# Kernel tuning notes

Measured on AMD Instinct MI355X. Metric: run time of the kernel, lower is better.

Reference implementation:

```python
import jax, jax.numpy as jnp
import numpy as np
import math

B, T = 8, 16
CODE_NUM = 1024
CODE_SIZE = 48
GRAPH_SIZE = 32
HIDDEN = 150      # hidden_size == t_output_size
T_ATTN = 32       # t_attention_size
DP_ATTN = 32      # DotProductAttention size
OUT = 1024


def _lin(k, fan_in, fan_out):
    s = 1.0 / math.sqrt(fan_in)
    kw, kb = jax.random.split(k)
    W = jax.random.uniform(kw, (fan_in, fan_out), minval=-s, maxval=s, dtype=jnp.float32)
    b = jax.random.uniform(kb, (fan_out,), minval=-s, maxval=s, dtype=jnp.float32)
    return W, b


def setup_inputs():
    key = jax.random.key(0)
    ks = jax.random.split(key, 16)
    u = jax.random.uniform(ks[0], (B, T, CODE_NUM))
    m1 = (u < 0.03).astype(jnp.float32)                   # persistent codes
    m2 = ((u >= 0.03) & (u < 0.05)).astype(jnp.float32)   # emerging neighbor codes
    m3 = ((u >= 0.05) & (u < 0.06)).astype(jnp.float32)   # emerging unrelated codes
    divided = jnp.stack([m1, m2, m3], axis=-1)            # [B,T,N,3], disjoint
    code_x = jnp.clip(m1 + m2 + m3, 0.0, 1.0)             # current-visit codes
    neighbors = ((u >= 0.06) & (u < 0.12)).astype(jnp.float32)
    lens = jax.random.randint(ks[1], (B,), T // 2, T + 1)
    a = (jax.random.uniform(ks[2], (CODE_NUM, CODE_NUM)) < 0.01).astype(jnp.float32)
    adj = a / (a.sum(axis=1, keepdims=True) + 1e-6)
    c_emb = jax.random.normal(ks[3], (CODE_NUM, CODE_SIZE)) * 0.05
    n_emb = jax.random.normal(ks[4], (CODE_NUM, CODE_SIZE)) * 0.05
    u_emb = jax.random.normal(ks[5], (CODE_NUM, GRAPH_SIZE)) * 0.05
    Wg, bg = _lin(ks[6], CODE_SIZE, GRAPH_SIZE)           # GraphLayer dense
    Wi, bi = _lin(ks[7], GRAPH_SIZE, 3 * HIDDEN)          # GRUCell input (r|z|n)
    Wh, bh = _lin(ks[8], HIDDEN, 3 * HIDDEN)              # GRUCell hidden (r|z|n)
    Wq, bq = _lin(ks[9], GRAPH_SIZE, T_ATTN)
    Wk, bk = _lin(ks[10], GRAPH_SIZE, T_ATTN)
    Wv, bv = _lin(ks[11], GRAPH_SIZE, HIDDEN)
    Wd, bd = _lin(ks[12], HIDDEN, DP_ATTN)                # DotProductAttention dense
    context = jax.random.normal(ks[13], (DP_ATTN,)) * 0.1
    Wc, bc = _lin(ks[14], HIDDEN, OUT)                    # Classifier
    return dict(code_x=code_x, divided=divided, neighbors=neighbors, lens=lens,
                adj=adj, c_emb=c_emb, n_emb=n_emb, u_emb=u_emb, Wg=Wg, bg=bg,
                Wi=Wi, bi=bi, Wh=Wh, bh=bh, Wq=Wq, bq=bq, Wk=Wk, bk=bk,
                Wv=Wv, bv=bv, Wd=Wd, bd=bd, context=context, Wc=Wc, bc=bc)


def _forward(code_x, divided, neighbors, lens, adj, c_emb, n_emb, u_emb,
             Wg, bg, Wi, bi, Wh, bh, Wq, bq, Wk, bk, Wv, bv, Wd, bd, context, Wc, bc):
    Bb, Tt, N = code_x.shape
    H = Wh.shape[0]
    NEG = -1e30
    scale = 1.0 / math.sqrt(Wq.shape[1])

    def step(carry, xs):
        h_prev, no_prev = carry                 # [B,N,H], [B,N,G]
        c_t, d_t, n_t, t_idx = xs               # [B,N], [B,N,3], [B,N], scalar
        c = c_t[..., None]
        nb = n_t[..., None]
        # GraphLayer: masked embeddings + one-hop adjacency aggregation
        ce = c * c_emb                           # [B,N,C]
        ne = nb * n_emb
        adj_ce = jnp.einsum('mn,bnc->bmc', adj, ce)
        adj_ne = jnp.einsum('mn,bnc->bmc', adj, ne)
        co = jax.nn.leaky_relu((ce + c * adj_ce + c * adj_ne) @ Wg + bg)      # [B,N,G]
        no = jax.nn.leaky_relu((ne + nb * adj_ne + nb * adj_ce) @ Wg + bg)

        m1 = d_t[..., 0]; m2 = d_t[..., 1]; m3 = d_t[..., 2]
        # TransitionLayer part 1: GRUCell on persistent (m1) codes; h_new starts at 0
        gi = co @ Wi + bi
        gh = h_prev @ Wh + bh
        i_r, i_z, i_n = jnp.split(gi, 3, axis=-1)
        h_r, h_z, h_n = jnp.split(gh, 3, axis=-1)
        r = jax.nn.sigmoid(i_r + h_r)
        z = jax.nn.sigmoid(i_z + h_z)
        n_g = jnp.tanh(i_n + r * h_n)
        h_m1 = (1.0 - z) * n_g + z * h_prev
        h_new = jnp.where(m1[..., None] > 0, h_m1, 0.0)

        # TransitionLayer part 2: single-head attention over emerging (m2|m3) codes, t>0
        m23 = (m2 + m3) > 0
        qrows = jnp.where(m2[..., None] > 0, no_prev,
                          jnp.where(m3[..., None] > 0, u_emb, 0.0))           # [B,N,G]
        q = qrows @ Wq + bq
        k = co @ Wk + bk
        v = qrows @ Wv + bv
        s = jnp.einsum('bia,bja->bij', q, k) * scale
        s = jnp.where(m23[:, None, :], s, NEG)   # keys restricted to m2|m3 set
        h_m23 = jnp.tanh(jnp.einsum('bij,bjh->bih', jax.nn.softmax(s, axis=-1), v))
        use23 = t_idx > 0
        h_new = jnp.where(jnp.logical_and(use23, m23)[..., None], h_m23, h_new)

        # per-step output: max-pool over each active subset (0 if subset empty)
        om1 = jnp.max(jnp.where(m1[..., None] > 0, h_m1, NEG), axis=1)
        om1 = jnp.where(jnp.any(m1 > 0, axis=1)[:, None], om1, 0.0)
        om23 = jnp.max(jnp.where(m23[..., None], h_m23, NEG), axis=1)
        om23 = jnp.where(jnp.logical_and(use23, jnp.any(m23, axis=1))[:, None], om23, 0.0)
        return (h_new, no), om1 + om23

    h0 = jnp.zeros((Bb, N, H), code_x.dtype)
    no0 = jnp.zeros((Bb, N, Wg.shape[1]), code_x.dtype)
    xs = (jnp.moveaxis(code_x, 1, 0), jnp.moveaxis(divided, 1, 0),
          jnp.moveaxis(neighbors, 1, 0), jnp.arange(Tt))
    _, outs = jax.lax.scan(step, (h0, no0), xs)
    outs = jnp.moveaxis(outs, 0, 1)              # [B,T,H]

    # DotProductAttention over (ragged) visit axis
    vu = (outs @ Wd + bd) @ context              # [B,T]
    tmask = jnp.arange(Tt)[None, :] < lens[:, None]
    score = jax.nn.softmax(jnp.where(tmask, vu, NEG), axis=-1)
    pooled = jnp.einsum('bth,bt->bh', outs, score)
    # Classifier (dropout_rate=0 -> identity) with sigmoid activation
    return jax.nn.sigmoid(pooled @ Wc + bc)


def reference(code_x, divided, neighbors, lens, adj, c_emb, n_emb, u_emb,
              Wg, bg, Wi, bi, Wh, bh, Wq, bq, Wk, bk, Wv, bv, Wd, bd, context, Wc, bc):
    return _forward(code_x, divided, neighbors, lens, adj, c_emb, n_emb, u_emb,
                    Wg, bg, Wi, bi, Wh, bh, Wq, bq, Wk, bk, Wv, bv, Wd, bd,
                    context, Wc, bc)
```

## Files before the change

### kernel.cpp

```cpp
#include <hip/hip_runtime.h>

#define Bq   8
#define Tq   16
#define Nq   1024
#define Cq   48
#define Gq   32
#define Hq   150
#define H3q  450
#define TAq  32
#define OUTq 1024
#define BTq  128
#define NBLK (2 * BTq)
#define THREADS 512

#define NC_CAP 128
#define NM_CAP 64
#define NACT   (2 * NC_CAP)
#define MTILE  16
#define NMH    (NM_CAP / 2)
#define CHUNK  16

__device__ __forceinline__ float lrelu(float x){ return x > 0.f ? x : 0.01f * x; }
__device__ __forceinline__ float sigm(float x){ return 1.f / (1.f + expf(-x)); }

__device__ __align__(16) int   g_n1[BTq], g_n23[BTq], g_nchain[BTq], g_nchain2[BTq];
__device__ __align__(16) int   g_list1[BTq][NM_CAP];
__device__ __align__(16) int   g_list23[BTq][NM_CAP];
__device__ __align__(16) int   g_mapc[BTq][Nq];
__device__ __align__(16) int   g_mapn[BTq][Nq];
__device__ __align__(16) int   g_chain[BTq][NM_CAP];
__device__ __align__(16) int   g_chain2[BTq][NM_CAP];
__device__ __align__(16) int   g_cls[BTq][NM_CAP];
__device__ __align__(16) float g_co[BTq][NC_CAP][Gq];
__device__ __align__(16) float g_no[BTq][NC_CAP][Gq];
__device__ __align__(16) float g_hm23[BTq][NM_CAP][Hq];
__device__ __align__(16) float g_om23p2[2][BTq][Hq];
__device__ __align__(16) float g_hm1[BTq][NM_CAP][Hq];
__device__ __align__(16) float g_om1p2[2][BTq][Hq];
__device__ __align__(16) float g_om1c[BTq][Hq];

template<typename T>
__device__ __forceinline__ T gld(const T* p){
    return __hip_atomic_load(p, __ATOMIC_RELAXED, __HIP_MEMORY_SCOPE_AGENT);
}
template<typename T>
__device__ __forceinline__ void gst(T* p, T v){
    __hip_atomic_store(p, v, __ATOMIC_RELAXED, __HIP_MEMORY_SCOPE_AGENT);
}

__device__ unsigned int g_done[NBLK][16];

__device__ __forceinline__ void publish(unsigned int val){
    asm volatile("s_waitcnt vmcnt(0)" ::: "memory");
    __syncthreads();
    if (threadIdx.x == 0)
        __hip_atomic_store(&g_done[blockIdx.x][0], val,
                           __ATOMIC_RELAXED, __HIP_MEMORY_SCOPE_AGENT);
}

__device__ __forceinline__ void spin_ge(int b2, unsigned int tgt){
    while ((int)(__hip_atomic_load(&g_done[b2][0],
                                   __ATOMIC_RELAXED, __HIP_MEMORY_SCOPE_AGENT) - tgt) < 0)
        __builtin_amdgcn_s_sleep(4);
}

__device__ __forceinline__ void gi3(const float* co_row, const float* Wi, const float* bi, int h,
                                    float& gr, float& gz, float& gn){
    gr = bi[h]; gz = bi[Hq + h]; gn = bi[2 * Hq + h];
    #pragma unroll
    for (int g = 0; g < Gq; ++g){
        float c = co_row[g];
        const float* w = Wi + g * H3q + h;
        gr += c * w[0];
        gz += c * w[Hq];
        gn += c * w[2 * Hq];
    }
}

#define WARM(ptr, nfloats) { int nv_ = (nfloats) >> 2; \
    for (int i4_ = blk * THREADS + tid; i4_ < nv_; i4_ += NBLK * THREADS){ \
        float4 v_ = ((const float4*)(ptr))[i4_]; \
        wacc += v_.x + v_.y + v_.z + v_.w; } }

union SharedU {
    struct {
        unsigned char cf[Nq], nf[Nq];
        short lc[NC_CAP], ln[NC_CAP];
        short act[NACT];
        float Wg[Cq][Gq];
        float Pact[NACT][Gq];
        float A[MTILE][NACT];
    } co;
    struct {
        unsigned char f1[Nq], f2[Nq], f3[Nq];
        short l1[NM_CAP], l23[NM_CAP];
        unsigned char wm[NMH];
        float co23[NM_CAP][Gq];
        float qr[NM_CAP][Gq];
        float q[NMH][TAq + 1];
        float k[NM_CAP][TAq + 1];
        float s[NMH][NM_CAP + 1];
        float vv[NM_CAP][Hq];
        float hm[NMH][Hq];
    } mid;
    struct {
        short map1p[Nq], map23p[Nq];
        short l1[NM_CAP];
        unsigned char cls[NM_CAP];
        int   m23l[NM_CAP];
        float co1[NMH][Gq];
        float hb[Hq];
        float ghf[H3q];
        float gi[NMH][H3q];
    } g1;
    struct {
        int   proc[NM_CAP];
        float hb[CHUNK][Hq];
        float co[CHUNK][Gq];
        float ghf[CHUNK][H3q];
        float hm[CHUNK][Hq];
        float cmax[Hq];
    } g1b;
    struct {
        int   nch2[Tq];
        float co[Gq];
        float hb[Hq];
        float ghf[H3q];
        float outs[Tq][Hq];
        float wdc[Hq];
        float score[Tq];
        float pooled[Hq];
    } fin;
};

#define CO_PREFETCH(P, kk) { int rbase_ = half + (kk) * 2 * MTILE; \
    int ntile_ = min(MTILE, (total - rbase_ + 1) / 2); int lim_ = ntile_ * total; \
    _Pragma("unroll") for (int u = 0; u < 8; ++u){ int idx_ = tid + u * THREADS; \
        if (idx_ < lim_){ int ti_ = idx_ / total, j_ = idx_ - ti_ * total; \
            P[u] = adj[(size_t)sh.co.act[rbase_ + 2 * ti_] * Nq + sh.co.act[j_]]; } } }

#define CO_STORE(P, kk) { int rbase_ = half + (kk) * 2 * MTILE; \
    int ntile_ = min(MTILE, (total - rbase_ + 1) / 2); int lim_ = ntile_ * total; \
    _Pragma("unroll") for (int u = 0; u < 8; ++u){ int idx_ = tid + u * THREADS; \
        if (idx_ < lim_){ int ti_ = idx_ / total, j_ = idx_ - ti_ * total; \
            sh.co.A[ti_][j_] = P[u]; } } }

#define CO_COMPUTE(kk) { int rbase_ = half + (kk) * 2 * MTILE; \
    int ntile_ = min(MTILE, (total - rbase_ + 1) / 2); \
    if (grp < ntile_){ int r_ = rbase_ + 2 * grp; float agg_ = 0.f; \
        _Pragma("unroll 4") for (int j_ = 0; j_ < total; ++j_) \
            agg_ += sh.co.A[grp][j_] * sh.co.Pact[j_][g]; \
        float v_ = lrelu(sh.co.Pact[r_][g] + agg_ + bgv); \
        if (r_ < nc) gst(&g_co[bt][r_][g], v_); else gst(&g_no[bt][r_ - nc][g], v_); } }

__global__ __launch_bounds__(THREADS, 1) void k_fused(
    const float* code_x, const float* divided, const float* neighbors,
    const int* lens, const float* adj, const float* c_emb, const float* n_emb,
    const float* u_emb, const float* Wg, const float* bg,
    const float* Wi, const float* bi, const float* Wh, const float* bh,
    const float* Wq_, const float* bq_, const float* Wk_, const float* bk_,
    const float* Wv_, const float* bv_, const float* Wd, const float* bd,
    const float* ctx, const float* Wc, const float* bc, float* out)
{
    __shared__ SharedU sh;
    __shared__ int s_n0, s_n1v, s_i2;
    const int tid = threadIdx.x;
    const int blk = blockIdx.x;
    const int bt   = blk >> 1;
    const int half = blk & 1;
    const int t    = bt % Tq;
    const int btp  = bt - 1;
    const unsigned int bar0 = __hip_atomic_load(&g_done[blk][0],
                                                __ATOMIC_RELAXED, __HIP_MEMORY_SCOPE_AGENT);

    float wacc = 0.f;
    WARM(code_x,    BTq * Nq);
    WARM(neighbors, BTq * Nq);
    WARM(adj,       Nq * Nq);
    WARM(divided,   BTq * Nq * 3);
    WARM(c_emb,     Nq * Cq);
    WARM(n_emb,     Nq * Cq);
    WARM(u_emb,     Nq * Gq);
    WARM(Wi,        Gq * H3q);
    WARM(Wh,        Hq * H3q);
    WARM(Wc,        Hq * OUTq);
    WARM(Wv_,       Gq * Hq);
    WARM(Wd,        Hq * TAq);
    WARM((const float*)g_co,     BTq * NC_CAP * Gq);
    WARM((const float*)g_no,     BTq * NC_CAP * Gq);
    WARM((const float*)g_hm23,   BTq * NM_CAP * Hq);
    WARM((const float*)g_hm1,    BTq * NM_CAP * Hq);
    WARM((const float*)g_mapc,   BTq * Nq);
    WARM((const float*)g_mapn,   BTq * Nq);
    WARM((const float*)g_om23p2, 2 * BTq * Hq);
    WARM((const float*)g_om1p2,  2 * BTq * Hq);
    WARM((const float*)g_om1c,   BTq * Hq);

    {
        int wave = tid >> 6, lane = tid & 63;
        for (int n = tid; n < Nq; n += THREADS){
            sh.co.cf[n] = (code_x[bt * Nq + n]    > 0.f) ? 1 : 0;
            sh.co.nf[n] = (neighbors[bt * Nq + n] > 0.f) ? 1 : 0;
        }
        for (int i = tid; i < Cq * Gq; i += THREADS) (&sh.co.Wg[0][0])[i] = Wg[i];
        __syncthreads();
        if (wave == 0){
            int base = 0;
            for (int start = 0; start < Nq; start += 64){
                int n = start + lane;
                int pred = sh.co.cf[n];
                unsigned long long mm = __ballot(pred != 0);
                int pos = base + (int)__popcll(mm & ((1ull << lane) - 1ull));
                if (pred && pos < NC_CAP) sh.co.lc[pos] = (short)n;
                base += (int)__popcll(mm);
            }
            if (lane == 0) s_n0 = min(base, NC_CAP);
        } else if (wave == 1){
            int base = 0;
            for (int start = 0; start < Nq; start += 64){
                int n = start + lane;
                int pred = sh.co.nf[n];
                unsigned long long mm = __ballot(pred != 0);
                int pos = base + (int)__popcll(mm & ((1ull << lane) - 1ull));
                if (pred && pos < NC_CAP) sh.co.ln[pos] = (short)n;
                base += (int)__popcll(mm);
            }
            if (lane == 0) s_n1v = min(base, NC_CAP);
        } else {
            if (half == 0) for (int n = tid - 128; n < Nq; n += 384) gst(&g_mapc[bt][n], -1);
            else           for (int n = tid - 128; n < Nq; n += 384) gst(&g_mapn[bt][n], -1);
        }
        __syncthreads();
        int nc = s_n0, nn = s_n1v, total = nc + nn;

        for (int i = tid; i < total; i += THREADS) sh.co.act[i] = (i < nc) ? sh.co.lc[i] : sh.co.ln[i - nc];
        if (half == 0) for (int i = tid; i < nc; i += THREADS) gst(&g_mapc[bt][sh.co.lc[i]], i);
        else           for (int i = tid; i < nn; i += THREADS) gst(&g_mapn[bt][sh.co.ln[i]], i);
        __syncthreads();

        for (int idx = tid; idx < total * Gq; idx += THREADS){
            int i = idx >> 5, g = idx & 31;
            int row = sh.co.act[i];
            const float* e = (i < nc) ? (c_emb + row * Cq) : (n_emb + row * Cq);
            float acc = 0.f;
            #pragma unroll
            for (int c = 0; c < Cq; ++c) acc += e[c] * sh.co.Wg[c][g];
            sh.co.Pact[i][g] = acc;
        }
        __syncthreads();

        int g = tid & 31, grp = tid >> 5;
        float bgv = bg[g];
        int ntiles = (total > half) ? (total - half + 2 * MTILE - 1) / (2 * MTILE) : 0;
        float pA[8], pB[8];
        if (ntiles > 0) CO_PREFETCH(pA, 0);
        for (int k = 0; k < ntiles; ){
            CO_STORE(pA, k);
            __syncthreads();
            if (k + 1 < ntiles) CO_PREFETCH(pB, k + 1);
            CO_COMPUTE(k);
            __syncthreads();
            ++k; if (k >= ntiles) break;
            CO_STORE(pB, k);
            __syncthreads();
            if (k + 1 < ntiles) CO_PREFETCH(pA, k + 1);
            CO_COMPUTE(k);
            __syncthreads();
            ++k;
        }
    }
    asm volatile("" :: "v"(wacc));
    publish(bar0 + 1);
    float dv[6];
    #pragma unroll
    for (int u = 0; u < 6; ++u) dv[u] = divided[(size_t)bt * (Nq * 3) + tid + u * THREADS];
    if (tid == 0) spin_ge(blk ^ 1, bar0 + 1);
    else if (t > 0 && tid == 1) spin_ge(2 * btp,     bar0 + 1);
    else if (t > 0 && tid == 2) spin_ge(2 * btp + 1, bar0 + 1);
    __syncthreads();

    {
        int wave = tid >> 6, lane = tid & 63;
        #pragma unroll
        for (int u = 0; u < 6; ++u){
            int idx = tid + u * THREADS;
            int n = idx / 3, c = idx - n * 3;
            unsigned char f = (dv[u] > 0.f) ? 1 : 0;
            if (c == 0) sh.mid.f1[n] = f;
            else if (c == 1) sh.mid.f2[n] = f;
            else sh.mid.f3[n] = f;
        }
        __syncthreads();
        if (wave == 0){
            int base = 0;
            for (int start = 0; start < Nq; start += 64){
                int n = start + lane;
                int pred = sh.mid.f1[n];
                unsigned long long mm = __ballot(pred != 0);
                int pos = base + (int)__popcll(mm & ((1ull << lane) - 1ull));
                if (pred && pos < NM_CAP) sh.mid.l1[pos] = (short)n;
                base += (int)__popcll(mm);
            }
            if (lane == 0) s_n0 = min(base, NM_CAP);
        } else if (wave == 1){
            int base = 0;
            for (int start = 0; start < Nq; start += 64){
                int n = start + lane;
                int m2 = sh.mid.f2[n], m3 = sh.mid.f3[n];
                int pred = m2 | m3;
                unsigned long long mm = __ballot(pred != 0);
                int pos = base + (int)__popcll(mm & ((1ull << lane) - 1ull));
                if (pred && pos < NM_CAP) sh.mid.l23[pos] = (short)(n | (m2 ? 0x400 : 0));
                base += (int)__popcll(mm);
            }
            if (lane == 0) s_n1v = min(base, NM_CAP);
        }
        __syncthreads();
        int n1 = s_n0, n23 = s_n1v;
        if (half == 0){
            for (int i = tid; i < n1;  i += THREADS) gst(&g_list1[bt][i],  (int)sh.mid.l1[i]);
            for (int i = tid; i < n23; i += THREADS) gst(&g_list23[bt][i], (int)sh.mid.l23[i]);
            if (tid == 0){ gst(&g_n1[bt], n1); gst(&g_n23[bt], n23); }
        }
        if (t != 0 && n23 != 0){
            int nMy = (n23 > half) ? ((n23 - half + 1) >> 1) : 0;

            for (int il = tid; il < nMy; il += THREADS){
                int row = sh.mid.l23[2 * il + half] & 1023;
                unsigned char wmv = 0;
                if (t < Tq - 1) wmv = (divided[((size_t)(bt + 1) * Nq + row) * 3] > 0.f) ? 1 : 0;
                sh.mid.wm[il] = wmv;
            }
            for (int idx = tid; idx < n23 * Gq; idx += THREADS){
                int i = idx >> 5, g = idx & 31;
                sh.mid.co23[i][g] = gld(&g_co[bt][gld(&g_mapc[bt][sh.mid.l23[i] & 1023])][g]);
            }
            for (int idx = tid; idx < n23 * Gq; idx += THREADS){
                int i = idx >> 5, g = idx & 31;
                int e = sh.mid.l23[i], row = e & 1023;
                float qv;
                if (e & 0x400){
                    int slot = gld(&g_mapn[btp][row]);
                    qv = (slot >= 0) ? gld(&g_no[btp][slot][g]) : lrelu(bg[g]);
                } else {
                    qv = u_emb[row * Gq + g];
                }
                sh.mid.qr[i][g] = qv;
            }
            __syncthreads();
            for (int idx = tid; idx < n23 * TAq; idx += THREADS){
                int i = idx >> 5, a = idx & 31;
                float acck = bk_[a];
                #pragma unroll
                for (int g = 0; g < Gq; ++g) acck += sh.mid.co23[i][g] * Wk_[g * TAq + a];
                sh.mid.k[i][a] = acck;
            }
            for (int idx = tid; idx < nMy * TAq; idx += THREADS){
                int il = idx >> 5, a = idx & 31;
                int i = 2 * il + half;
                float accq = bq_[a];
                #pragma unroll
                for (int g = 0; g < Gq; ++g) accq += sh.mid.qr[i][g] * Wq_[g * TAq + a];
                sh.mid.q[il][a] = accq;
            }
            for (int idx = tid; idx < n23 * Hq; idx += THREADS){
                int i = idx / Hq, h = idx % Hq;
                float acc = bv_[h];
                #pragma unroll
                for (int g = 0; g < Gq; ++g) acc += sh.mid.qr[i][g] * Wv_[g * Hq + h];
                sh.mid.vv[i][h] = acc;
            }
            __syncthreads();

            const float scale = 0.17677669529663687f;
            for (int idx = tid; idx < nMy * n23; idx += THREADS){
                int il = idx / n23, j = idx % n23;
                float acc = 0.f;
                #pragma unroll
                for (int a = 0; a < TAq; ++a) acc += sh.mid.q[il][a] * sh.mid.k[j][a];
                sh.mid.s[il][j] = acc * scale;
            }
            __syncthreads();
            for (int il = tid; il < nMy; il += THREADS){
                float mx = -1e30f;
                for (int j = 0; j < n23; ++j) mx = fmaxf(mx, sh.mid.s[il][j]);
                float sum = 0.f;
                for (int j = 0; j < n23; ++j){ float e = expf(sh.mid.s[il][j] - mx); sh.mid.s[il][j] = e; sum += e; }
                float inv = 1.f / sum;
                for (int j = 0; j < n23; ++j) sh.mid.s[il][j] *= inv;
            }
            __syncthreads();
            for (int idx = tid; idx < nMy * Hq; idx += THREADS){
                int il = idx / Hq, h = idx % Hq;
                float acc = 0.f;
                for (int j = 0; j < n23; ++j) acc += sh.mid.s[il][j] * sh.mid.vv[j][h];
                sh.mid.hm[il][h] = tanhf(acc);
            }
            __syncthreads();
            for (int idx = tid; idx < nMy * Hq; idx += THREADS){
                int il = idx / Hq, h = idx % Hq;
                if (sh.mid.wm[il]) gst(&g_hm23[bt][2 * il + half][h], sh.mid.hm[il][h]);
            }
            for (int h = tid; h < Hq; h += THREADS){
                float mx = -1e30f;
                for (int il = 0; il < nMy; ++il) mx = fmaxf(mx, sh.mid.hm[il][h]);
                gst(&g_om23p2[half][bt][h], mx);
            }
        }
    }
    publish(bar0 + 2);
    if (tid == 0) spin_ge(blk ^ 1, bar0 + 2);
    else if (t > 0 && tid == 1) spin_ge(2 * btp,     bar0 + 2);
    else if (t > 0 && tid == 2) spin_ge(2 * btp + 1, bar0 + 2);
    __syncthreads();

    {
        int n1 = gld(&g_n1[bt]);
        int nMy = (n1 > half) ? ((n1 - half + 1) >> 1) : 0;
        for (int n = tid; n < Nq; n += THREADS){
            if (t >= 1) sh.g1.map1p[n] = -1;
            if (t >= 2) sh.g1.map23p[n] = -1;
        }
        for (int i = tid; i < n1; i += THREADS) sh.g1.l1[i] = (short)gld(&g_list1[bt][i]);
        __syncthreads();
        if (t >= 1){
            int n1p = gld(&g_n1[btp]);
            for (int i = tid; i < n1p; i += THREADS) sh.g1.map1p[gld(&g_list1[btp][i])] = (short)i;
            if (t >= 2){
                int n23p = gld(&g_n23[btp]);
                for (int i = tid; i < n23p; i += THREADS) sh.g1.map23p[gld(&g_list23[btp][i]) & 1023] = (short)i;
            }
        }
        __syncthreads();
        if (tid < 64){
            int i = tid;
            int cls = 0, sp = -1;
            if (i < n1 && t >= 1){
                int row = sh.g1.l1[i];
                if (sh.g1.map1p[row] >= 0){ cls = 1; sp = sh.g1.map1p[row]; }
                else if (t >= 2 && sh.g1.map23p[row] >= 0){ cls = 2; sp = sh.g1.map23p[row]; }
            }
            if (i < n1) sh.g1.cls[i] = (unsigned char)cls;
            if (half == 0 && i < n1) gst(&g_cls[bt][i], cls);
            unsigned long long mch = __ballot(cls == 1);
            unsigned long long m23 = __ballot(cls == 2 && (i & 1) == half);
            int pch = (int)__popcll(mch & ((1ull << i) - 1ull));
            int p23 = (int)__popcll(m23 & ((1ull << i) - 1ull));
            if (half == 0 && cls == 1) gst(&g_chain[bt][pch], (i << 16) | sp);
            if (cls == 2 && (i & 1) == half) sh.g1.m23l[p23] = (i << 16) | sp;
            if (i == 0){
                s_i2 = (int)__popcll(m23);
                if (half == 0) gst(&g_nchain[bt], (int)__popcll(mch));
            }
        }
        for (int idx = tid; idx < nMy * Gq; idx += THREADS){
            int il = idx >> 5, g = idx & 31;
            sh.g1.co1[il][g] = gld(&g_co[bt][gld(&g_mapc[bt][sh.g1.l1[2 * il + half]])][g]);
        }
        __syncthreads();

        if (tid < H3q){
            float wcol[Gq];
            #pragma unroll
            for (int g = 0; g < Gq; ++g) wcol[g] = Wi[g * H3q + tid];
            float bij = bi[tid];
            for (int il = 0; il < nMy; ++il){
                float acc = bij;
                #pragma unroll
                for (int g = 0; g < Gq; ++g) acc += sh.g1.co1[il][g] * wcol[g];
                sh.g1.gi[il][tid] = acc;
            }
        }
        __syncthreads();

        for (int idx = tid; idx < nMy * Hq; idx += THREADS){
            int il = idx / Hq, h = idx % Hq;
            int i = 2 * il + half;
            if (sh.g1.cls[i] != 0) continue;
            float gr = sh.g1.gi[il][h], gz = sh.g1.gi[il][Hq + h], gn = sh.g1.gi[il][2 * Hq + h];
            float r  = sigm(gr + bh[h]);
            float z  = sigm(gz + bh[Hq + h]);
            float ng = tanhf(gn + r * bh[2 * Hq + h]);
            sh.g1.gi[il][h] = (1.f - z) * ng;
        }
        __syncthreads();

        int nf23 = s_i2;
        for (int f = 0; f < nf23; ++f){
            int pk = sh.g1.m23l[f]; int i = pk >> 16, sp = pk & 0xffff;
            int il = i >> 1;
            for (int h = tid; h < Hq; h += THREADS) sh.g1.hb[h] = gld(&g_hm23[btp][sp][h]);
            __syncthreads();
            for (int j = tid; j < H3q; j += THREADS){
                float acc = bh[j];
                for (int k2 = 0; k2 < Hq; ++k2) acc += sh.g1.hb[k2] * Wh[k2 * H3q + j];
                sh.g1.ghf[j] = acc;
            }
            __syncthreads();
            for (int h = tid; h < Hq; h += THREADS){
                float gr = sh.g1.gi[il][h], gz = sh.g1.gi[il][Hq + h], gn = sh.g1.gi[il][2 * Hq + h];
                float r  = sigm(gr + sh.g1.ghf[h]);
                float z  = sigm(gz + sh.g1.ghf[Hq + h]);
                float ng = tanhf(gn + r * sh.g1.ghf[2 * Hq + h]);
                sh.g1.gi[il][h] = (1.f - z) * ng + z * sh.g1.hb[h];
            }
            __syncthreads();
        }

        for (int idx = tid; idx < nMy * Hq; idx += THREADS){
            int il = idx / Hq, h = idx % Hq;
            int i = 2 * il + half;
            if (sh.g1.cls[i] != 1) gst(&g_hm1[bt][i][h], sh.g1.gi[il][h]);
        }
        for (int h = tid; h < Hq; h += THREADS){
            float mx = -1e30f;
            for (int il = 0; il < nMy; ++il)
                if (sh.g1.cls[2 * il + half] != 1) mx = fmaxf(mx, sh.g1.gi[il][h]);
            gst(&g_om1p2[half][bt][h], mx);
        }
    }

    if (half == 1){
        publish(bar0 + 5);
        return;
    }
    publish(bar0 + 3);
    if (t > 0){
        if (tid == 0) spin_ge(2 * btp,     bar0 + 3);
        else if (tid == 1) spin_ge(2 * btp + 1, bar0 + 3);
    }
    __syncthreads();

    {
        int nch = (t > 0) ? gld(&g_nchain[bt]) : 0;
        for (int h = tid; h < Hq; h += THREADS) sh.g1b.cmax[h] = -1e30f;
        if (tid < 64){
            int c = tid;
            int pk = 0, defer = 0;
            if (c < nch){
                pk = gld(&g_chain[bt][c]);
                int sp = pk & 0xffff;
                defer = (gld(&g_cls[btp][sp]) == 1) ? 1 : 0;
            }
            unsigned long long md = __ballot((c < nch) && defer);
            unsigned long long mp = __ballot((c < nch) && !defer);
            int pos  = (int)__popcll(md & ((1ull << c) - 1ull));
            int ppos = (int)__popcll(mp & ((1ull << c) - 1ull));
            if ((c < nch) && defer)  gst(&g_chain2[bt][pos], pk);
            if ((c < nch) && !defer) sh.g1b.proc[ppos] = pk;
            if (c == 0){
                gst(&g_nchain2[bt], (int)__popcll(md));
                s_i2 = (int)__popcll(mp);
            }
        }
        __syncthreads();
        int nproc = s_i2;
        for (int cb = 0; cb < nproc; cb += CHUNK){
            int nc2 = min(CHUNK, nproc - cb);
            for (int idx = tid; idx < nc2 * Hq; idx += THREADS){
                int c = idx / Hq, h = idx % Hq;
                int sp = sh.g1b.proc[cb + c] & 0xffff;
                sh.g1b.hb[c][h] = gld(&g_hm1[btp][sp][h]);
            }
            for (int idx = tid; idx < nc2 * Gq; idx += THREADS){
                int c = idx >> 5, g = idx & 31;
                int i = sh.g1b.proc[cb + c] >> 16;
                sh.g1b.co[c][g] = gld(&g_co[bt][gld(&g_mapc[bt][gld(&g_list1[bt][i])])][g]);
            }
            __syncthreads();
            for (int idx = tid; idx < nc2 * H3q; idx += THREADS){
                int c = idx / H3q, j = idx - c * H3q;
                float acc = bh[j];
                for (int k2 = 0; k2 < Hq; ++k2) acc += sh.g1b.hb[c][k2] * Wh[k2 * H3q + j];
                sh.g1b.ghf[c][j] = acc;
            }
            __syncthreads();
            for (int idx = tid; idx < nc2 * Hq; idx += THREADS){
                int c = idx / Hq, h = idx % Hq;
                int i = sh.g1b.proc[cb + c] >> 16;
                float gr, gz, gn;
                gi3(sh.g1b.co[c], Wi, bi, h, gr, gz, gn);
                float r  = sigm(gr + sh.g1b.ghf[c][h]);
                float z  = sigm(gz + sh.g1b.ghf[c][Hq + h]);
                float ng = tanhf(gn + r * sh.g1b.ghf[c][2 * Hq + h]);
                float v  = (1.f - z) * ng + z * sh.g1b.hb[c][h];
                gst(&g_hm1[bt][i][h], v);
                sh.g1b.hm[c][h] = v;
            }
            __syncthreads();
            for (int h = tid; h < Hq; h += THREADS){
                float mx = sh.g1b.cmax[h];
                for (int c = 0; c < nc2; ++c) mx = fmaxf(mx, sh.g1b.hm[c][h]);
                sh.g1b.cmax[h] = mx;
            }
            __syncthreads();
        }
        for (int h = tid; h < Hq; h += THREADS) gst(&g_om1c[bt][h], sh.g1b.cmax[h]);
    }

    if ((blk & 31) != 0){
        publish(bar0 + 5);
        return;
    }
    publish(bar0 + 4);
    {
        int b = blk >> 5;
        if (tid < 32){
            int tt = tid >> 1, par = tid & 1;
            spin_ge(32 * b + 2 * tt + par, par ? (bar0 + 3) : (bar0 + 4));
        }
    }
    __syncthreads();

    {
        int b = blk >> 5;
        if (tid < Tq) sh.fin.nch2[tid] = (tid > 0) ? gld(&g_nchain2[b * Tq + tid]) : 0;
        __syncthreads();
        for (int tt = 1; tt < Tq; ++tt){
            int bt2 = b * Tq + tt, btp2 = bt2 - 1;
            int nch2 = sh.fin.nch2[tt];
            for (int c = 0; c < nch2; ++c){
                int pk = gld(&g_chain2[bt2][c]); int i = pk >> 16, sp = pk & 0xffff;
                if (tid < Gq) sh.fin.co[tid] = gld(&g_co[bt2][gld(&g_mapc[bt2][gld(&g_list1[bt2][i])])][tid]);
                for (int h = tid; h < Hq; h += THREADS) sh.fin.hb[h] = gld(&g_hm1[btp2][sp][h]);
                __syncthreads();
                for (int j = tid; j < H3q; j += THREADS){
                    float acc = bh[j];
                    for (int k2 = 0; k2 < Hq; ++k2) acc += sh.fin.hb[k2] * Wh[k2 * H3q + j];
                    sh.fin.ghf[j] = acc;
                }
                __syncthreads();
                for (int h = tid; h < Hq; h += THREADS){
                    float gr, gz, gn;
                    gi3(sh.fin.co, Wi, bi, h, gr, gz, gn);
                    float r  = sigm(gr + sh.fin.ghf[h]);
                    float z  = sigm(gz + sh.fin.ghf[Hq + h]);
                    float ng = tanhf(gn + r * sh.fin.ghf[2 * Hq + h]);
                    gst(&g_hm1[bt2][i][h], (1.f - z) * ng + z * sh.fin.hb[h]);
                }
                __syncthreads();
            }
        }
        for (int idx = tid; idx < Tq * Hq; idx += THREADS){
            int tt = idx / Hq, h = idx % Hq;
            int bt2 = b * Tq + tt;
            int n1 = gld(&g_n1[bt2]), n23 = (tt > 0) ? gld(&g_n23[bt2]) : 0;
            float o = 0.f;
            if (n1 > 0){
                float mx = fmaxf(fmaxf(gld(&g_om1p2[0][bt2][h]), gld(&g_om1p2[1][bt2][h])),
                                 gld(&g_om1c[bt2][h]));
                int nd = sh.fin.nch2[tt];
                for (int c = 0; c < nd; ++c){
                    int i = gld(&g_chain2[bt2][c]) >> 16;
                    mx = fmaxf(mx, gld(&g_hm1[bt2][i][h]));
                }
                o = mx;
            }
            if (n23 > 0) o += fmaxf(gld(&g_om23p2[0][bt2][h]), gld(&g_om23p2[1][bt2][h]));
            sh.fin.outs[tt][h] = o;
        }
        for (int h = tid; h < Hq; h += THREADS){
            float acc = 0.f;
            for (int d = 0; d < 32; ++d) acc += Wd[h * 32 + d] * ctx[d];
            sh.fin.wdc[h] = acc;
        }
        __syncthreads();
        int len = lens[b];
        if (tid < Tq){
            int tt = tid;
            float acc = 0.f;
            for (int d = 0; d < 32; ++d) acc += bd[d] * ctx[d];
            for (int h = 0; h < Hq; ++h) acc += sh.fin.outs[tt][h] * sh.fin.wdc[h];
            sh.fin.score[tt] = (tt < len) ? acc : -1e30f;
        }
        __syncthreads();
        if (tid == 0){
            float mx = -1e30f;
            for (int tt = 0; tt < Tq; ++tt) mx = fmaxf(mx, sh.fin.score[tt]);
            float sum = 0.f;
            for (int tt = 0; tt < Tq; ++tt){ float e = expf(sh.fin.score[tt] - mx); sh.fin.score[tt] = e; sum += e; }
            float inv = 1.f / sum;
            for (int tt = 0; tt < Tq; ++tt) sh.fin.score[tt] *= inv;
        }
        __syncthreads();
        for (int h = tid; h < Hq; h += THREADS){
            float acc = 0.f;
            for (int tt = 0; tt < Tq; ++tt) acc += sh.fin.score[tt] * sh.fin.outs[tt][h];
            sh.fin.pooled[h] = acc;
        }
        __syncthreads();
        for (int o = tid; o < OUTq; o += THREADS){
            float acc = bc[o];
            for (int h = 0; h < Hq; ++h) acc += sh.fin.pooled[h] * Wc[h * OUTq + o];
            out[b * OUTq + o] = sigm(acc);
        }
    }
    publish(bar0 + 5);
}

extern "C" void kernel_launch(void* const* d_in, const int* in_sizes, int n_in,
                              void* d_out, int out_size, void* d_ws, size_t ws_size,
                              hipStream_t stream){
    const float* code_x    = (const float*)d_in[0];
    const float* divided   = (const float*)d_in[1];
    const float* neighbors = (const float*)d_in[2];
    const int*   lens      = (const int*)  d_in[3];
    const float* adj       = (const float*)d_in[4];
    const float* c_emb     = (const float*)d_in[5];
    const float* n_emb     = (const float*)d_in[6];
    const float* u_emb     = (const float*)d_in[7];
    const float* Wg        = (const float*)d_in[8];
    const float* bg        = (const float*)d_in[9];
    const float* Wi        = (const float*)d_in[10];
    const float* bi        = (const float*)d_in[11];
    const float* Wh        = (const float*)d_in[12];
    const float* bh        = (const float*)d_in[13];
    const float* Wq_       = (const float*)d_in[14];
    const float* bq_       = (const float*)d_in[15];
    const float* Wk_       = (const float*)d_in[16];
    const float* bk_       = (const float*)d_in[17];
    const float* Wv_       = (const float*)d_in[18];
    const float* bv_       = (const float*)d_in[19];
    const float* Wd_       = (const float*)d_in[20];
    const float* bd_       = (const float*)d_in[21];
    const float* ctx       = (const float*)d_in[22];
    const float* Wc_       = (const float*)d_in[23];
    const float* bc_       = (const float*)d_in[24];
    float* out = (float*)d_out;

    hipLaunchKernelGGL(k_fused, dim3(NBLK), dim3(THREADS), 0, stream,
                       code_x, divided, neighbors, lens, adj, c_emb, n_emb, u_emb,
                       Wg, bg, Wi, bi, Wh, bh, Wq_, bq_, Wk_, bk_, Wv_, bv_,
                       Wd_, bd_, ctx, Wc_, bc_, out);
}
```

Before: 237.1 us.

## Distribute final attention and classifier across all blocks per batch

Previously a single block per batch element ran the pooling and the full 1024-wide classifier while the other blocks exited. Now every block of a batch recomputes the attention pooling and produces its own 32-output slice of the classifier, with a split-K reduction through shared memory. The deferred-chain GRU pass stays on the leader block, which publishes a new barrier that the others wait on. Warm-up prefetches of the workspace buffers are also removed. The cost is redundant pooling work in every block and an extra cross-block wait stage.

```diff
diff --git a/kernel.cpp b/kernel.cpp
--- a/kernel.cpp
+++ b/kernel.cpp
@@ -130,6 +130,7 @@
         float wdc[Hq];
         float score[Tq];
         float pooled[Hq];
+        float cpart[32][17];
     } fin;
 };
 
@@ -186,15 +187,6 @@
     WARM(Wc,        Hq * OUTq);
     WARM(Wv_,       Gq * Hq);
     WARM(Wd,        Hq * TAq);
-    WARM((const float*)g_co,     BTq * NC_CAP * Gq);
-    WARM((const float*)g_no,     BTq * NC_CAP * Gq);
-    WARM((const float*)g_hm23,   BTq * NM_CAP * Hq);
-    WARM((const float*)g_hm1,    BTq * NM_CAP * Hq);
-    WARM((const float*)g_mapc,   BTq * Nq);
-    WARM((const float*)g_mapn,   BTq * Nq);
-    WARM((const float*)g_om23p2, 2 * BTq * Hq);
-    WARM((const float*)g_om1p2,  2 * BTq * Hq);
-    WARM((const float*)g_om1c,   BTq * Hq);
 
     {
         int wave = tid >> 6, lane = tid & 63;
@@ -519,128 +511,125 @@
             gst(&g_om1p2[half][bt][h], mx);
         }
     }
-
-    if (half == 1){
-        publish(bar0 + 5);
-        return;
+    publish(bar0 + 3);
+
+    if (half == 0){
+        if (t > 0){
+            if (tid == 0) spin_ge(2 * btp,     bar0 + 3);
+            else if (tid == 1) spin_ge(2 * btp + 1, bar0 + 3);
+        }
+        __syncthreads();
+        {
+            int nch = (t > 0) ? gld(&g_nchain[bt]) : 0;
+            for (int h = tid; h < Hq; h += THREADS) sh.g1b.cmax[h] = -1e30f;
+            if (tid < 64){
+                int c = tid;
+                int pk = 0, defer = 0;
+                if (c < nch){
+                    pk = gld(&g_chain[bt][c]);
+                    int sp = pk & 0xffff;
+                    defer = (gld(&g_cls[btp][sp]) == 1) ? 1 : 0;
+                }
+                unsigned long long md = __ballot((c < nch) && defer);
+                unsigned long long mp = __ballot((c < nch) && !defer);
+                int pos  = (int)__popcll(md & ((1ull << c) - 1ull));
+                int ppos = (int)__popcll(mp & ((1ull << c) - 1ull));
+                if ((c < nch) && defer)  gst(&g_chain2[bt][pos], pk);
+                if ((c < nch) && !defer) sh.g1b.proc[ppos] = pk;
+                if (c == 0){
+                    gst(&g_nchain2[bt], (int)__popcll(md));
+                    s_i2 = (int)__popcll(mp);
+                }
+            }
+            __syncthreads();
+            int nproc = s_i2;
+            for (int cb = 0; cb < nproc; cb += CHUNK){
+                int nc2 = min(CHUNK, nproc - cb);
+                for (int idx = tid; idx < nc2 * Hq; idx += THREADS){
+                    int c = idx / Hq, h = idx % Hq;
+                    int sp = sh.g1b.proc[cb + c] & 0xffff;
+                    sh.g1b.hb[c][h] = gld(&g_hm1[btp][sp][h]);
+                }
+                for (int idx = tid; idx < nc2 * Gq; idx += THREADS){
+                    int c = idx >> 5, g = idx & 31;
+                    int i = sh.g1b.proc[cb + c] >> 16;
+                    sh.g1b.co[c][g] = gld(&g_co[bt][gld(&g_mapc[bt][gld(&g_list1[bt][i])])][g]);
+                }
+                __syncthreads();
+                for (int idx = tid; idx < nc2 * H3q; idx += THREADS){
+                    int c = idx / H3q, j = idx - c * H3q;
+                    float acc = bh[j];
+                    for (int k2 = 0; k2 < Hq; ++k2) acc += sh.g1b.hb[c][k2] * Wh[k2 * H3q + j];
+                    sh.g1b.ghf[c][j] = acc;
+                }
+                __syncthreads();
+                for (int idx = tid; idx < nc2 * Hq; idx += THREADS){
+                    int c = idx / Hq, h = idx % Hq;
+                    int i = sh.g1b.proc[cb + c] >> 16;
+                    float gr, gz, gn;
+                    gi3(sh.g1b.co[c], Wi, bi, h, gr, gz, gn);
+                    float r  = sigm(gr + sh.g1b.ghf[c][h]);
+                    float z  = sigm(gz + sh.g1b.ghf[c][Hq + h]);
+                    float ng = tanhf(gn + r * sh.g1b.ghf[c][2 * Hq + h]);
+                    float v  = (1.f - z) * ng + z * sh.g1b.hb[c][h];
+                    gst(&g_hm1[bt][i][h], v);
+                    sh.g1b.hm[c][h] = v;
+                }
+                __syncthreads();
+                for (int h = tid; h < Hq; h += THREADS){
+                    float mx = sh.g1b.cmax[h];
+                    for (int c = 0; c < nc2; ++c) mx = fmaxf(mx, sh.g1b.hm[c][h]);
+                    sh.g1b.cmax[h] = mx;
+                }
+                __syncthreads();
+            }
+            for (int h = tid; h < Hq; h += THREADS) gst(&g_om1c[bt][h], sh.g1b.cmax[h]);
+        }
+        publish(bar0 + 4);
+
+        if ((blk & 31) == 0){
+            int b = blk >> 5;
+            if (tid < 16) spin_ge(32 * b + 2 * tid, bar0 + 4);
+            __syncthreads();
+            if (tid < Tq) sh.fin.nch2[tid] = (tid > 0) ? gld(&g_nchain2[b * Tq + tid]) : 0;
+            __syncthreads();
+            for (int tt = 1; tt < Tq; ++tt){
+                int bt2 = b * Tq + tt, btp2 = bt2 - 1;
+                int nch2 = sh.fin.nch2[tt];
+                for (int c = 0; c < nch2; ++c){
+                    int pk = gld(&g_chain2[bt2][c]); int i = pk >> 16, sp = pk & 0xffff;
+                    if (tid < Gq) sh.fin.co[tid] = gld(&g_co[bt2][gld(&g_mapc[bt2][gld(&g_list1[bt2][i])])][tid]);
+                    for (int h = tid; h < Hq; h += THREADS) sh.fin.hb[h] = gld(&g_hm1[btp2][sp][h]);
+                    __syncthreads();
+                    for (int j = tid; j < H3q; j += THREADS){
+                        float acc = bh[j];
+                        for (int k2 = 0; k2 < Hq; ++k2) acc += sh.fin.hb[k2] * Wh[k2 * H3q + j];
+                        sh.fin.ghf[j] = acc;
+                    }
+                    __syncthreads();
+                    for (int h = tid; h < Hq; h += THREADS){
+                        float gr, gz, gn;
+                        gi3(sh.fin.co, Wi, bi, h, gr, gz, gn);
+                        float r  = sigm(gr + sh.fin.ghf[h]);
+                        float z  = sigm(gz + sh.fin.ghf[Hq + h]);
+                        float ng = tanhf(gn + r * sh.fin.ghf[2 * Hq + h]);
+                        gst(&g_hm1[bt2][i][h], (1.f - z) * ng + z * sh.fin.hb[h]);
+                    }
+                    __syncthreads();
+                }
+            }
+            publish(bar0 + 5);
+        }
     }
-    publish(bar0 + 3);
-    if (t > 0){
-        if (tid == 0) spin_ge(2 * btp,     bar0 + 3);
-        else if (tid == 1) spin_ge(2 * btp + 1, bar0 + 3);
-    }
-    __syncthreads();
-
-    {
-        int nch = (t > 0) ? gld(&g_nchain[bt]) : 0;
-        for (int h = tid; h < Hq; h += THREADS) sh.g1b.cmax[h] = -1e30f;
-        if (tid < 64){
-            int c = tid;
-            int pk = 0, defer = 0;
-            if (c < nch){
-                pk = gld(&g_chain[bt][c]);
-                int sp = pk & 0xffff;
-                defer = (gld(&g_cls[btp][sp]) == 1) ? 1 : 0;
-            }
-            unsigned long long md = __ballot((c < nch) && defer);
-            unsigned long long mp = __ballot((c < nch) && !defer);
-            int pos  = (int)__popcll(md & ((1ull << c) - 1ull));
-            int ppos = (int)__popcll(mp & ((1ull << c) - 1ull));
-            if ((c < nch) && defer)  gst(&g_chain2[bt][pos], pk);
-            if ((c < nch) && !defer) sh.g1b.proc[ppos] = pk;
-            if (c == 0){
-                gst(&g_nchain2[bt], (int)__popcll(md));
-                s_i2 = (int)__popcll(mp);
-            }
-        }
-        __syncthreads();
-        int nproc = s_i2;
-        for (int cb = 0; cb < nproc; cb += CHUNK){
-            int nc2 = min(CHUNK, nproc - cb);
-            for (int idx = tid; idx < nc2 * Hq; idx += THREADS){
-                int c = idx / Hq, h = idx % Hq;
-                int sp = sh.g1b.proc[cb + c] & 0xffff;
-                sh.g1b.hb[c][h] = gld(&g_hm1[btp][sp][h]);
-            }
-            for (int idx = tid; idx < nc2 * Gq; idx += THREADS){
-                int c = idx >> 5, g = idx & 31;
-                int i = sh.g1b.proc[cb + c] >> 16;
-                sh.g1b.co[c][g] = gld(&g_co[bt][gld(&g_mapc[bt][gld(&g_list1[bt][i])])][g]);
-            }
-            __syncthreads();
-            for (int idx = tid; idx < nc2 * H3q; idx += THREADS){
-                int c = idx / H3q, j = idx - c * H3q;
-                float acc = bh[j];
-                for (int k2 = 0; k2 < Hq; ++k2) acc += sh.g1b.hb[c][k2] * Wh[k2 * H3q + j];
-                sh.g1b.ghf[c][j] = acc;
-            }
-            __syncthreads();
-            for (int idx = tid; idx < nc2 * Hq; idx += THREADS){
-                int c = idx / Hq, h = idx % Hq;
-                int i = sh.g1b.proc[cb + c] >> 16;
-                float gr, gz, gn;
-                gi3(sh.g1b.co[c], Wi, bi, h, gr, gz, gn);
-                float r  = sigm(gr + sh.g1b.ghf[c][h]);
-                float z  = sigm(gz + sh.g1b.ghf[c][Hq + h]);
-                float ng = tanhf(gn + r * sh.g1b.ghf[c][2 * Hq + h]);
-                float v  = (1.f - z) * ng + z * sh.g1b.hb[c][h];
-                gst(&g_hm1[bt][i][h], v);
-                sh.g1b.hm[c][h] = v;
-            }
-            __syncthreads();
-            for (int h = tid; h < Hq; h += THREADS){
-                float mx = sh.g1b.cmax[h];
-                for (int c = 0; c < nc2; ++c) mx = fmaxf(mx, sh.g1b.hm[c][h]);
-                sh.g1b.cmax[h] = mx;
-            }
-            __syncthreads();
-        }
-        for (int h = tid; h < Hq; h += THREADS) gst(&g_om1c[bt][h], sh.g1b.cmax[h]);
-    }
-
-    if ((blk & 31) != 0){
-        publish(bar0 + 5);
-        return;
-    }
-    publish(bar0 + 4);
+
     {
         int b = blk >> 5;
-        if (tid < 32){
-            int tt = tid >> 1, par = tid & 1;
-            spin_ge(32 * b + 2 * tt + par, par ? (bar0 + 3) : (bar0 + 4));
-        }
-    }
-    __syncthreads();
-
-    {
-        int b = blk >> 5;
+        if (tid == 0) spin_ge(32 * b, bar0 + 5);
+        else if (tid >= 1 && tid < 17) spin_ge(32 * b + 2 * (tid - 1) + 1, bar0 + 3);
+        __syncthreads();
+
         if (tid < Tq) sh.fin.nch2[tid] = (tid > 0) ? gld(&g_nchain2[b * Tq + tid]) : 0;
         __syncthreads();
-        for (int tt = 1; tt < Tq; ++tt){
-            int bt2 = b * Tq + tt, btp2 = bt2 - 1;
-            int nch2 = sh.fin.nch2[tt];
-            for (int c = 0; c < nch2; ++c){
-                int pk = gld(&g_chain2[bt2][c]); int i = pk >> 16, sp = pk & 0xffff;
-                if (tid < Gq) sh.fin.co[tid] = gld(&g_co[bt2][gld(&g_mapc[bt2][gld(&g_list1[bt2][i])])][tid]);
-                for (int h = tid; h < Hq; h += THREADS) sh.fin.hb[h] = gld(&g_hm1[btp2][sp][h]);
-                __syncthreads();
-                for (int j = tid; j < H3q; j += THREADS){
-                    float acc = bh[j];
-                    for (int k2 = 0; k2 < Hq; ++k2) acc += sh.fin.hb[k2] * Wh[k2 * H3q + j];
-                    sh.fin.ghf[j] = acc;
-                }
-                __syncthreads();
-                for (int h = tid; h < Hq; h += THREADS){
-                    float gr, gz, gn;
-                    gi3(sh.fin.co, Wi, bi, h, gr, gz, gn);
-                    float r  = sigm(gr + sh.fin.ghf[h]);
-                    float z  = sigm(gz + sh.fin.ghf[Hq + h]);
-                    float ng = tanhf(gn + r * sh.fin.ghf[2 * Hq + h]);
-                    gst(&g_hm1[bt2][i][h], (1.f - z) * ng + z * sh.fin.hb[h]);
-                }
-                __syncthreads();
-            }
-        }
         for (int idx = tid; idx < Tq * Hq; idx += THREADS){
             int tt = idx / Hq, h = idx % Hq;
             int bt2 = b * Tq + tt;
@@ -689,13 +678,24 @@
             sh.fin.pooled[h] = acc;
         }
         __syncthreads();
-        for (int o = tid; o < OUTq; o += THREADS){
+        int obase = (blk & 31) * 32;
+        {
+            int ol = tid & 31, seg = tid >> 5;
+            int h0 = seg * 10, h1 = min(Hq, h0 + 10);
+            float acc = 0.f;
+            for (int h = h0; h < h1; ++h) acc += sh.fin.pooled[h] * Wc[h * OUTq + obase + ol];
+            sh.fin.cpart[ol][seg] = acc;
+        }
+        __syncthreads();
+        if (tid < 32){
+            int o = obase + tid;
             float acc = bc[o];
-            for (int h = 0; h < Hq; ++h) acc += sh.fin.pooled[h] * Wc[h * OUTq + o];
+            #pragma unroll
+            for (int s2 = 0; s2 < 16; ++s2) acc += sh.fin.cpart[tid][s2];
             out[b * OUTq + o] = sigm(acc);
         }
     }
-    publish(bar0 + 5);
+    publish(bar0 + 6);
 }
 
 extern "C" void kernel_launch(void* const* d_in, const int* in_sizes, int n_in,
```

Result: no change. 233.3 us, median of 3 (-1.6%).
